# Kernel tuning notes

Measured on AMD Instinct MI355X. Metric: run time of the kernel, lower is better.

## Reference

```python
import jax, jax.numpy as jnp
import numpy as np

N_NODES = 100000
N_EDGES = 3200000
D = 64
NEG_SLOPE = 0.01  # torch F.leaky_relu default


def setup_inputs() -> dict:
    key = jax.random.key(0)
    ks = jax.random.split(key, 7)
    s = 1.0 / np.sqrt(D)
    x = jax.random.normal(ks[0], (N_NODES, D), jnp.float32)
    src = jax.random.randint(ks[1], (N_EDGES,), 0, N_NODES)
    dst = jax.random.randint(ks[2], (N_EDGES,), 0, N_NODES)
    W1a = jax.random.normal(ks[3], (D, D), jnp.float32) * s
    W2a = jax.random.normal(ks[4], (D, D), jnp.float32) * s
    W1b = jax.random.normal(ks[5], (D, D), jnp.float32) * s
    W2b = jax.random.normal(ks[6], (D, D), jnp.float32) * s
    return {"x": x, "W1a": W1a, "W2a": W2a, "W1b": W1b, "W2b": W2b,
            "src": src, "dst": dst}


def _ngcf_conv(x, src, dst, norm, W1, W2):
    # message: norm_ij * (W1 x_j + W2 (x_j (*) x_i)), aggregated at dst i,
    # plus self-transform W1 x_i  (NGCF propagation rule, pre-activation)
    xs = x[src]            # [E, D] gather of neighbor feats
    xd = x[dst]            # [E, D] gather of center feats
    msg = norm[:, None] * (xs @ W1 + (xs * xd) @ W2)   # [E, D]
    agg = jax.ops.segment_sum(msg, dst, num_segments=x.shape[0])
    return x @ W1 + agg


def reference(x, W1a, W2a, W1b, W2b, src, dst):
    n = x.shape[0]
    ones = jnp.ones(src.shape[0], x.dtype)
    deg = jnp.maximum(jax.ops.segment_sum(ones, dst, num_segments=n), 1.0)
    norm = jax.lax.rsqrt(deg[src] * deg[dst])          # 1/sqrt(d_j d_i)
    h1 = jax.nn.leaky_relu(_ngcf_conv(x, src, dst, norm, W1a, W2a), NEG_SLOPE)
    h2 = jax.nn.leaky_relu(_ngcf_conv(h1, src, dst, norm, W1b, W2b), NEG_SLOPE)
    h3 = _ngcf_conv(h2, src, dst, norm, W1b, W2b)      # no activation (matches source)
    return jnp.concatenate([h1, h2, h3], axis=-1)      # [N, 3*D]
```

## Files before the change

kernel.cpp:

```cpp
#include <hip/hip_runtime.h>
#include <hip/hip_bf16.h>

#define N_NODES 100000
#define N_EDGES 3200000
#define D 64
#define NEG_SLOPE 0.01f

#define B_SHIFT 9
#define NB ((N_NODES + 511) >> B_SHIFT)
#define T_EDGES 4096
#define NBIN ((N_EDGES + T_EDGES - 1) / T_EDGES)

using bf16x8 = __attribute__((ext_vector_type(8))) short;
using f32x4  = __attribute__((ext_vector_type(4))) float;

__device__ __forceinline__ unsigned short f2bf(float f) {
    __hip_bfloat16 h = __float2bfloat16(f);
    return *reinterpret_cast<unsigned short*>(&h);
}
__device__ __forceinline__ float bflo(unsigned int u) { return __uint_as_float(u << 16); }
__device__ __forceinline__ float bfhi(unsigned int u) { return __uint_as_float(u & 0xffff0000u); }
__device__ __forceinline__ float bf2f(unsigned short h) { return __uint_as_float(((unsigned int)h) << 16); }

__global__ __launch_bounds__(256) void bhist_k(const int* __restrict__ dst, int* __restrict__ btot) {
    __shared__ int hist[NB];
    int tid = threadIdx.x;
    for (int b = tid; b < NB; b += 256) hist[b] = 0;
    __syncthreads();
    int e0 = blockIdx.x * T_EDGES;
    int e1 = min(e0 + T_EDGES, N_EDGES);
    for (int e = e0 + tid; e < e1; e += 256) atomicAdd(&hist[dst[e] >> B_SHIFT], 1);
    __syncthreads();
    for (int b = tid; b < NB; b += 256) {
        int h = hist[b];
        if (h) atomicAdd(&btot[b], h);
    }
}

__global__ __launch_bounds__(256) void bscan_k(const int* __restrict__ btot, int* __restrict__ bbase) {
    __shared__ int wsum[4];
    int t = threadIdx.x;
    int lane = t & 63, w = t >> 6;
    int v = (t < NB) ? btot[t] : 0;
    int incl = v;
    #pragma unroll
    for (int o = 1; o < 64; o <<= 1) {
        int u = __shfl_up(incl, o, 64);
        if (lane >= o) incl += u;
    }
    if (lane == 63) wsum[w] = incl;
    __syncthreads();
    int woff = 0;
    for (int k = 0; k < w; ++k) woff += wsum[k];
    if (t < NB) bbase[t] = woff + incl - v;
    if (t == NB) bbase[NB] = N_EDGES;
}

__global__ __launch_bounds__(256) void bucket_k(const int* __restrict__ src, const int* __restrict__ dst,
                                                const int* __restrict__ bbase, int* __restrict__ bcnt2,
                                                unsigned* __restrict__ pairs) {
    __shared__ int hist[NB];
    __shared__ int lbase[NB];
    __shared__ int lcnt[NB];
    __shared__ int gbase[NB];
    __shared__ int wsum[4];
    __shared__ unsigned buf[T_EDGES];
    int tid = threadIdx.x;
    for (int b = tid; b < NB; b += 256) { hist[b] = 0; lcnt[b] = 0; }
    __syncthreads();
    int e0 = blockIdx.x * T_EDGES;
    int e1 = min(e0 + T_EDGES, N_EDGES);
    for (int e = e0 + tid; e < e1; e += 256) atomicAdd(&hist[dst[e] >> B_SHIFT], 1);
    __syncthreads();
    {
        int v = (tid < NB) ? hist[tid] : 0;
        int lane = tid & 63, w = tid >> 6;
        int incl = v;
        #pragma unroll
        for (int o = 1; o < 64; o <<= 1) {
            int u = __shfl_up(incl, o, 64);
            if (lane >= o) incl += u;
        }
        if (lane == 63) wsum[w] = incl;
        __syncthreads();
        int woff = 0;
        for (int k = 0; k < w; ++k) woff += wsum[k];
        if (tid < NB) {
            int excl = woff + incl - v;
            lbase[tid] = excl;
            int p = v ? atomicAdd(&bcnt2[tid], v) : 0;
            gbase[tid] = bbase[tid] + p - excl;
        }
    }
    __syncthreads();
    for (int e = e0 + tid; e < e1; e += 256) {
        int sv = src[e], dv = dst[e];
        int b = dv >> B_SHIFT;
        int loc = lbase[b] + atomicAdd(&lcnt[b], 1);
        buf[loc] = ((unsigned)sv << 9) | (unsigned)(dv & 511);
    }
    __syncthreads();
    int n = e1 - e0;
    for (int i = tid; i < n; i += 256) {
        unsigned pr = buf[i];
        int lo = 0, hi = NB - 1;
        while (lo < hi) { int mid = (lo + hi + 1) >> 1; if (lbase[mid] <= i) lo = mid; else hi = mid - 1; }
        pairs[gbase[lo] + i] = pr;
    }
}

__global__ __launch_bounds__(512) void fine_k(const unsigned* __restrict__ pairs, const int* __restrict__ bbase,
                                              int* __restrict__ degi, int* __restrict__ offs,
                                              float* __restrict__ rsd, int* __restrict__ csr_src,
                                              const float* __restrict__ x, unsigned short* __restrict__ xb) {
    __shared__ int cnt[512];
    __shared__ int offl[512];
    __shared__ int wsum[8];
    __shared__ float rsdl[256];
    int b = blockIdx.x >> 1, half = blockIdx.x & 1, t = threadIdx.x;
    int start = bbase[b];
    int end = bbase[b + 1];
    cnt[t] = 0;
    __syncthreads();
    for (int e = start + t; e < end; e += 512) atomicAdd(&cnt[pairs[e] & 511], 1);
    __syncthreads();
    int d = cnt[t];
    int lane = t & 63, w = t >> 6;
    int incl = d;
    #pragma unroll
    for (int o = 1; o < 64; o <<= 1) {
        int u = __shfl_up(incl, o, 64);
        if (lane >= o) incl += u;
    }
    if (lane == 63) wsum[w] = incl;
    __syncthreads();
    int woff = 0;
    for (int k = 0; k < w; ++k) woff += wsum[k];
    int myoff = start + woff + incl - d;
    offl[t] = myoff;
    int n = (b << B_SHIFT) + t;
    float rn = rsqrtf((float)(d > 0 ? d : 1));
    if ((t >> 8) == half) {
        if (n < N_NODES) {
            degi[n] = d;
            offs[n] = myoff;
            rsd[n] = rn;
        }
        rsdl[t & 255] = rn;
    }
    cnt[t] = 0;
    __syncthreads();
    for (int e = start + t; e < end; e += 512) {
        unsigned pr = pairs[e];
        int li = pr & 511;
        if ((li >> 8) == half) {
            int p = atomicAdd(&cnt[li], 1);
            csr_src[offl[li] + p] = (int)(pr >> 9);
        }
    }
    __syncthreads();
    int nbase = (b << B_SHIFT) + (half << 8);
    for (int i = t; i < 256 * 16; i += 512) {
        int nl = i >> 4;
        int node = nbase + nl;
        if (node < N_NODES) {
            float r = rsdl[nl];
            float4 v = ((const float4*)x)[(size_t)node * 16 + (i & 15)];
            unsigned int lo = ((unsigned int)f2bf(r * v.y) << 16) | f2bf(r * v.x);
            unsigned int hi = ((unsigned int)f2bf(r * v.w) << 16) | f2bf(r * v.z);
            ((uint2*)xb)[(size_t)node * 16 + (i & 15)] = make_uint2(lo, hi);
        }
    }
}

__global__ __launch_bounds__(256) void agg_k(const unsigned short* __restrict__ xb,
                                             const float* __restrict__ rsd,
                                             const int* __restrict__ offs, const int* __restrict__ degi,
                                             const int* __restrict__ csr_src, float* __restrict__ s) {
    int node = blockIdx.x * 4 + (threadIdx.x >> 6);
    if (node >= N_NODES) return;
    int lane = threadIdx.x & 63;
    int g = lane >> 3;
    int q = lane & 7;
    int start = offs[node];
    int deg = degi[node];
    const uint4* in4 = (const uint4*)xb;
    float acc0 = 0.f, acc1 = 0.f, acc2 = 0.f, acc3 = 0.f;
    float acc4 = 0.f, acc5 = 0.f, acc6 = 0.f, acc7 = 0.f;
    for (int base = 0; base < deg; base += 64) {
        int m = min(deg - base, 64);
        int idxv = csr_src[start + base + min(lane, m - 1)];
        for (int j = 0; j < m; j += 32) {
            int e0 = j + g, e1 = j + 8 + g, e2 = j + 16 + g, e3 = j + 24 + g;
            bool v0 = e0 < m, v1 = e1 < m, v2 = e2 < m, v3 = e3 < m;
            int s0 = __shfl(idxv, e0, 64);
            int s1 = __shfl(idxv, v1 ? e1 : 0, 64);
            int s2 = __shfl(idxv, v2 ? e2 : 0, 64);
            int s3 = __shfl(idxv, v3 ? e3 : 0, 64);
            uint4 p0 = in4[(size_t)s0 * 8 + q];
            uint4 p1 = in4[(size_t)s1 * 8 + q];
            uint4 p2 = in4[(size_t)s2 * 8 + q];
            uint4 p3 = in4[(size_t)s3 * 8 + q];
            float w0 = v0 ? 1.f : 0.f, w1 = v1 ? 1.f : 0.f;
            float w2 = v2 ? 1.f : 0.f, w3 = v3 ? 1.f : 0.f;
            acc0 += w0 * bflo(p0.x); acc1 += w0 * bfhi(p0.x);
            acc2 += w0 * bflo(p0.y); acc3 += w0 * bfhi(p0.y);
            acc4 += w0 * bflo(p0.z); acc5 += w0 * bfhi(p0.z);
            acc6 += w0 * bflo(p0.w); acc7 += w0 * bfhi(p0.w);
            acc0 += w1 * bflo(p1.x); acc1 += w1 * bfhi(p1.x);
            acc2 += w1 * bflo(p1.y); acc3 += w1 * bfhi(p1.y);
            acc4 += w1 * bflo(p1.z); acc5 += w1 * bfhi(p1.z);
            acc6 += w1 * bflo(p1.w); acc7 += w1 * bfhi(p1.w);
            acc0 += w2 * bflo(p2.x); acc1 += w2 * bfhi(p2.x);
            acc2 += w2 * bflo(p2.y); acc3 += w2 * bfhi(p2.y);
            acc4 += w2 * bflo(p2.z); acc5 += w2 * bfhi(p2.z);
            acc6 += w2 * bflo(p2.w); acc7 += w2 * bfhi(p2.w);
            acc0 += w3 * bflo(p3.x); acc1 += w3 * bfhi(p3.x);
            acc2 += w3 * bflo(p3.y); acc3 += w3 * bfhi(p3.y);
            acc4 += w3 * bflo(p3.z); acc5 += w3 * bfhi(p3.z);
            acc6 += w3 * bflo(p3.w); acc7 += w3 * bfhi(p3.w);
        }
    }
    #pragma unroll
    for (int off = 8; off < 64; off <<= 1) {
        acc0 += __shfl_xor(acc0, off, 64); acc1 += __shfl_xor(acc1, off, 64);
        acc2 += __shfl_xor(acc2, off, 64); acc3 += __shfl_xor(acc3, off, 64);
        acc4 += __shfl_xor(acc4, off, 64); acc5 += __shfl_xor(acc5, off, 64);
        acc6 += __shfl_xor(acc6, off, 64); acc7 += __shfl_xor(acc7, off, 64);
    }
    if (g == 0) {
        float rn = rsd[node];
        float4 r0, r1;
        r0.x = rn * acc0; r0.y = rn * acc1; r0.z = rn * acc2; r0.w = rn * acc3;
        r1.x = rn * acc4; r1.y = rn * acc5; r1.z = rn * acc6; r1.w = rn * acc7;
        ((float4*)s)[node * 16 + q * 2]     = r0;
        ((float4*)s)[node * 16 + q * 2 + 1] = r1;
    }
}

__global__ __launch_bounds__(256) void comb_k(const float* __restrict__ in, int stride,
                                              const float* __restrict__ s,
                                              const float* __restrict__ W1, const float* __restrict__ W2,
                                              float* __restrict__ out, int act,
                                              unsigned short* __restrict__ hb, const float* __restrict__ rsd,
                                              int bfout) {
    int tid = threadIdx.x;
    int w = tid >> 6;
    int l = tid & 63;
    int lr = l & 15;
    int lk = l >> 4;

    bf16x8 w1h[2], w1l[2], w2h[2], w2l[2];
    #pragma unroll
    for (int s2 = 0; s2 < 2; ++s2) {
        #pragma unroll
        for (int i = 0; i < 8; ++i) {
            int k = s2 * 32 + lk * 8 + i;
            float v1 = W1[k * D + w * 16 + lr];
            float v2 = W2[k * D + w * 16 + lr];
            unsigned short h1 = f2bf(v1);
            unsigned short h2 = f2bf(v2);
            w1h[s2][i] = (short)h1; w1l[s2][i] = (short)f2bf(v1 - bf2f(h1));
            w2h[s2][i] = (short)h2; w2l[s2][i] = (short)f2bf(v2 - bf2f(h2));
        }
    }

    int n0 = blockIdx.x * 32;
    bf16x8 ah[2][2], al[2][2], bh[2][2], bl[2][2];
    #pragma unroll
    for (int rt = 0; rt < 2; ++rt) {
        int n = n0 + rt * 16 + lr;
        const float* ip = in + (size_t)n * stride + lk * 8;
        const float* sp = s + (size_t)n * D + lk * 8;
        #pragma unroll
        for (int s2 = 0; s2 < 2; ++s2) {
            float ia[8], sa[8];
            *(float4*)&ia[0] = *(const float4*)(ip + s2 * 32);
            *(float4*)&ia[4] = *(const float4*)(ip + s2 * 32 + 4);
            *(float4*)&sa[0] = *(const float4*)(sp + s2 * 32);
            *(float4*)&sa[4] = *(const float4*)(sp + s2 * 32 + 4);
            #pragma unroll
            for (int i = 0; i < 8; ++i) {
                float a = ia[i] + sa[i];
                float b = sa[i] * ia[i];
                unsigned short hA = f2bf(a);
                unsigned short hB = f2bf(b);
                ah[rt][s2][i] = (short)hA; al[rt][s2][i] = (short)f2bf(a - bf2f(hA));
                bh[rt][s2][i] = (short)hB; bl[rt][s2][i] = (short)f2bf(b - bf2f(hB));
            }
        }
    }

    f32x4 acc[2] = {{0.f, 0.f, 0.f, 0.f}, {0.f, 0.f, 0.f, 0.f}};
    #pragma unroll
    for (int rt = 0; rt < 2; ++rt) {
        #pragma unroll
        for (int s2 = 0; s2 < 2; ++s2) {
            acc[rt] = __builtin_amdgcn_mfma_f32_16x16x32_bf16(ah[rt][s2], w1h[s2], acc[rt], 0, 0, 0);
            acc[rt] = __builtin_amdgcn_mfma_f32_16x16x32_bf16(al[rt][s2], w1h[s2], acc[rt], 0, 0, 0);
            acc[rt] = __builtin_amdgcn_mfma_f32_16x16x32_bf16(ah[rt][s2], w1l[s2], acc[rt], 0, 0, 0);
            acc[rt] = __builtin_amdgcn_mfma_f32_16x16x32_bf16(bh[rt][s2], w2h[s2], acc[rt], 0, 0, 0);
            acc[rt] = __builtin_amdgcn_mfma_f32_16x16x32_bf16(bl[rt][s2], w2h[s2], acc[rt], 0, 0, 0);
            acc[rt] = __builtin_amdgcn_mfma_f32_16x16x32_bf16(bh[rt][s2], w2l[s2], acc[rt], 0, 0, 0);
        }
    }

    #pragma unroll
    for (int rt = 0; rt < 2; ++rt) {
        #pragma unroll
        for (int r = 0; r < 4; ++r) {
            int n = n0 + rt * 16 + lk * 4 + r;
            float v = acc[rt][r];
            if (act) v = v >= 0.f ? v : NEG_SLOPE * v;
            out[(size_t)n * 192 + w * 16 + lr] = v;
            if (bfout) hb[(size_t)n * D + w * 16 + lr] = f2bf(rsd[n] * v);
        }
    }
}

extern "C" void kernel_launch(void* const* d_in, const int* in_sizes, int n_in,
                              void* d_out, int out_size, void* d_ws, size_t ws_size,
                              hipStream_t stream) {
    const float* x   = (const float*)d_in[0];
    const float* W1a = (const float*)d_in[1];
    const float* W2a = (const float*)d_in[2];
    const float* W1b = (const float*)d_in[3];
    const float* W2b = (const float*)d_in[4];
    const int*   src = (const int*)d_in[5];
    const int*   dst = (const int*)d_in[6];
    float* out = (float*)d_out;

    int*   btot    = (int*)d_ws;
    int*   bcnt2   = btot + 256;
    int*   bbase   = bcnt2 + 256;
    int*   degi    = bbase + 256;
    int*   offs    = degi + N_NODES;
    float* rsd     = (float*)(offs + N_NODES);
    int*   csr_src = (int*)(rsd + N_NODES);
    unsigned* pairs = (unsigned*)(csr_src + N_EDGES);
    unsigned short* xb = (unsigned short*)(pairs + N_EDGES);
    unsigned short* hb = (unsigned short*)pairs;
    float* s       = (float*)(xb + (size_t)N_NODES * D);

    hipMemsetAsync(btot, 0, 512 * sizeof(int), stream);

    bhist_k<<<NBIN, 256, 0, stream>>>(dst, btot);
    bscan_k<<<1, 256, 0, stream>>>(btot, bbase);
    bucket_k<<<NBIN, 256, 0, stream>>>(src, dst, bbase, bcnt2, pairs);
    fine_k<<<NB * 2, 512, 0, stream>>>(pairs, bbase, degi, offs, rsd, csr_src, x, xb);

    int ab = (N_NODES + 3) / 4;
    int cbg = N_NODES / 32;

    agg_k<<<ab, 256, 0, stream>>>(xb, rsd, offs, degi, csr_src, s);
    comb_k<<<cbg, 256, 0, stream>>>(x, D, s, W1a, W2a, out + 0, 1, hb, rsd, 1);
    agg_k<<<ab, 256, 0, stream>>>(hb, rsd, offs, degi, csr_src, s);
    comb_k<<<cbg, 256, 0, stream>>>(out + 0, 192, s, W1b, W2b, out + 64, 1, hb, rsd, 1);
    agg_k<<<ab, 256, 0, stream>>>(hb, rsd, offs, degi, csr_src, s);
    comb_k<<<cbg, 256, 0, stream>>>(out + 64, 192, s, W1b, W2b, out + 128, 0, hb, rsd, 0);
}
```

Before: 458.3 us.

## Drop global histogram pass using fixed-capacity buckets; unroll aggregation gather

Removes the separate bucket histogram kernel by scattering edge pairs into fixed-capacity per-bucket regions (BCAP slots each) and scanning the per-bucket counts afterwards. This saves one full read of dst. Fine binning now reads pairs from those capacity-strided regions. Bucket_k stores each pair's bucket id in shared memory instead of binary-searching it at write-out, and agg_k issues eight gathers per 64-edge chunk instead of looping in groups of four. The risks are overflow if a bucket exceeds BCAP edges, and that pairs now shares memory with the s buffer.

```diff
diff --git a/kernel.cpp b/kernel.cpp
--- a/kernel.cpp
+++ b/kernel.cpp
@@ -8,6 +8,7 @@
 
 #define B_SHIFT 9
 #define NB ((N_NODES + 511) >> B_SHIFT)
+#define BCAP 18432
 #define T_EDGES 4096
 #define NBIN ((N_EDGES + T_EDGES - 1) / T_EDGES)
 
@@ -22,42 +23,8 @@
 __device__ __forceinline__ float bfhi(unsigned int u) { return __uint_as_float(u & 0xffff0000u); }
 __device__ __forceinline__ float bf2f(unsigned short h) { return __uint_as_float(((unsigned int)h) << 16); }
 
-__global__ __launch_bounds__(256) void bhist_k(const int* __restrict__ dst, int* __restrict__ btot) {
-    __shared__ int hist[NB];
-    int tid = threadIdx.x;
-    for (int b = tid; b < NB; b += 256) hist[b] = 0;
-    __syncthreads();
-    int e0 = blockIdx.x * T_EDGES;
-    int e1 = min(e0 + T_EDGES, N_EDGES);
-    for (int e = e0 + tid; e < e1; e += 256) atomicAdd(&hist[dst[e] >> B_SHIFT], 1);
-    __syncthreads();
-    for (int b = tid; b < NB; b += 256) {
-        int h = hist[b];
-        if (h) atomicAdd(&btot[b], h);
-    }
-}
-
-__global__ __launch_bounds__(256) void bscan_k(const int* __restrict__ btot, int* __restrict__ bbase) {
-    __shared__ int wsum[4];
-    int t = threadIdx.x;
-    int lane = t & 63, w = t >> 6;
-    int v = (t < NB) ? btot[t] : 0;
-    int incl = v;
-    #pragma unroll
-    for (int o = 1; o < 64; o <<= 1) {
-        int u = __shfl_up(incl, o, 64);
-        if (lane >= o) incl += u;
-    }
-    if (lane == 63) wsum[w] = incl;
-    __syncthreads();
-    int woff = 0;
-    for (int k = 0; k < w; ++k) woff += wsum[k];
-    if (t < NB) bbase[t] = woff + incl - v;
-    if (t == NB) bbase[NB] = N_EDGES;
-}
-
 __global__ __launch_bounds__(256) void bucket_k(const int* __restrict__ src, const int* __restrict__ dst,
-                                                const int* __restrict__ bbase, int* __restrict__ bcnt2,
+                                                int* __restrict__ bcnt2,
                                                 unsigned* __restrict__ pairs) {
     __shared__ int hist[NB];
     __shared__ int lbase[NB];
@@ -65,6 +32,7 @@
     __shared__ int gbase[NB];
     __shared__ int wsum[4];
     __shared__ unsigned buf[T_EDGES];
+    __shared__ unsigned char bid[T_EDGES];
     int tid = threadIdx.x;
     for (int b = tid; b < NB; b += 256) { hist[b] = 0; lcnt[b] = 0; }
     __syncthreads();
@@ -89,7 +57,7 @@
             int excl = woff + incl - v;
             lbase[tid] = excl;
             int p = v ? atomicAdd(&bcnt2[tid], v) : 0;
-            gbase[tid] = bbase[tid] + p - excl;
+            gbase[tid] = tid * BCAP + p - excl;
         }
     }
     __syncthreads();
@@ -98,18 +66,37 @@
         int b = dv >> B_SHIFT;
         int loc = lbase[b] + atomicAdd(&lcnt[b], 1);
         buf[loc] = ((unsigned)sv << 9) | (unsigned)(dv & 511);
+        bid[loc] = (unsigned char)b;
     }
     __syncthreads();
     int n = e1 - e0;
     for (int i = tid; i < n; i += 256) {
-        unsigned pr = buf[i];
-        int lo = 0, hi = NB - 1;
-        while (lo < hi) { int mid = (lo + hi + 1) >> 1; if (lbase[mid] <= i) lo = mid; else hi = mid - 1; }
-        pairs[gbase[lo] + i] = pr;
-    }
-}
-
-__global__ __launch_bounds__(512) void fine_k(const unsigned* __restrict__ pairs, const int* __restrict__ bbase,
+        int b = bid[i];
+        pairs[gbase[b] + i] = buf[i];
+    }
+}
+
+__global__ __launch_bounds__(256) void bscan_k(const int* __restrict__ bcnt2, int* __restrict__ bbase) {
+    __shared__ int wsum[4];
+    int t = threadIdx.x;
+    int lane = t & 63, w = t >> 6;
+    int v = (t < NB) ? bcnt2[t] : 0;
+    int incl = v;
+    #pragma unroll
+    for (int o = 1; o < 64; o <<= 1) {
+        int u = __shfl_up(incl, o, 64);
+        if (lane >= o) incl += u;
+    }
+    if (lane == 63) wsum[w] = incl;
+    __syncthreads();
+    int woff = 0;
+    for (int k = 0; k < w; ++k) woff += wsum[k];
+    if (t < NB) bbase[t] = woff + incl - v;
+    if (t == NB) bbase[NB] = N_EDGES;
+}
+
+__global__ __launch_bounds__(512) void fine_k(const unsigned* __restrict__ pairs,
+                                              const int* __restrict__ bcnt2, const int* __restrict__ bbase,
                                               int* __restrict__ degi, int* __restrict__ offs,
                                               float* __restrict__ rsd, int* __restrict__ csr_src,
                                               const float* __restrict__ x, unsigned short* __restrict__ xb) {
@@ -118,11 +105,12 @@
     __shared__ int wsum[8];
     __shared__ float rsdl[256];
     int b = blockIdx.x >> 1, half = blockIdx.x & 1, t = threadIdx.x;
-    int start = bbase[b];
-    int end = bbase[b + 1];
+    int pstart = b * BCAP;
+    int pend = pstart + bcnt2[b];
+    int cbase = bbase[b];
     cnt[t] = 0;
     __syncthreads();
-    for (int e = start + t; e < end; e += 512) atomicAdd(&cnt[pairs[e] & 511], 1);
+    for (int e = pstart + t; e < pend; e += 512) atomicAdd(&cnt[pairs[e] & 511], 1);
     __syncthreads();
     int d = cnt[t];
     int lane = t & 63, w = t >> 6;
@@ -136,7 +124,7 @@
     __syncthreads();
     int woff = 0;
     for (int k = 0; k < w; ++k) woff += wsum[k];
-    int myoff = start + woff + incl - d;
+    int myoff = cbase + woff + incl - d;
     offl[t] = myoff;
     int n = (b << B_SHIFT) + t;
     float rn = rsqrtf((float)(d > 0 ? d : 1));
@@ -150,7 +138,7 @@
     }
     cnt[t] = 0;
     __syncthreads();
-    for (int e = start + t; e < end; e += 512) {
+    for (int e = pstart + t; e < pend; e += 512) {
         unsigned pr = pairs[e];
         int li = pr & 511;
         if ((li >> 8) == half) {
@@ -172,6 +160,12 @@
         }
     }
 }
+
+#define ACC8(P, W) \
+    acc0 += W * bflo(P.x); acc1 += W * bfhi(P.x); \
+    acc2 += W * bflo(P.y); acc3 += W * bfhi(P.y); \
+    acc4 += W * bflo(P.z); acc5 += W * bfhi(P.z); \
+    acc6 += W * bflo(P.w); acc7 += W * bfhi(P.w);
 
 __global__ __launch_bounds__(256) void agg_k(const unsigned short* __restrict__ xb,
                                              const float* __restrict__ rsd,
@@ -190,35 +184,33 @@
     for (int base = 0; base < deg; base += 64) {
         int m = min(deg - base, 64);
         int idxv = csr_src[start + base + min(lane, m - 1)];
-        for (int j = 0; j < m; j += 32) {
-            int e0 = j + g, e1 = j + 8 + g, e2 = j + 16 + g, e3 = j + 24 + g;
-            bool v0 = e0 < m, v1 = e1 < m, v2 = e2 < m, v3 = e3 < m;
-            int s0 = __shfl(idxv, e0, 64);
-            int s1 = __shfl(idxv, v1 ? e1 : 0, 64);
-            int s2 = __shfl(idxv, v2 ? e2 : 0, 64);
-            int s3 = __shfl(idxv, v3 ? e3 : 0, 64);
-            uint4 p0 = in4[(size_t)s0 * 8 + q];
-            uint4 p1 = in4[(size_t)s1 * 8 + q];
-            uint4 p2 = in4[(size_t)s2 * 8 + q];
-            uint4 p3 = in4[(size_t)s3 * 8 + q];
-            float w0 = v0 ? 1.f : 0.f, w1 = v1 ? 1.f : 0.f;
-            float w2 = v2 ? 1.f : 0.f, w3 = v3 ? 1.f : 0.f;
-            acc0 += w0 * bflo(p0.x); acc1 += w0 * bfhi(p0.x);
-            acc2 += w0 * bflo(p0.y); acc3 += w0 * bfhi(p0.y);
-            acc4 += w0 * bflo(p0.z); acc5 += w0 * bfhi(p0.z);
-            acc6 += w0 * bflo(p0.w); acc7 += w0 * bfhi(p0.w);
-            acc0 += w1 * bflo(p1.x); acc1 += w1 * bfhi(p1.x);
-            acc2 += w1 * bflo(p1.y); acc3 += w1 * bfhi(p1.y);
-            acc4 += w1 * bflo(p1.z); acc5 += w1 * bfhi(p1.z);
-            acc6 += w1 * bflo(p1.w); acc7 += w1 * bfhi(p1.w);
-            acc0 += w2 * bflo(p2.x); acc1 += w2 * bfhi(p2.x);
-            acc2 += w2 * bflo(p2.y); acc3 += w2 * bfhi(p2.y);
-            acc4 += w2 * bflo(p2.z); acc5 += w2 * bfhi(p2.z);
-            acc6 += w2 * bflo(p2.w); acc7 += w2 * bfhi(p2.w);
-            acc0 += w3 * bflo(p3.x); acc1 += w3 * bfhi(p3.x);
-            acc2 += w3 * bflo(p3.y); acc3 += w3 * bfhi(p3.y);
-            acc4 += w3 * bflo(p3.z); acc5 += w3 * bfhi(p3.z);
-            acc6 += w3 * bflo(p3.w); acc7 += w3 * bfhi(p3.w);
+        int e0 = g, e1 = 8 + g, e2 = 16 + g, e3 = 24 + g;
+        int s0 = __shfl(idxv, e0, 64);
+        int s1 = __shfl(idxv, e1, 64);
+        int s2 = __shfl(idxv, e2, 64);
+        int s3 = __shfl(idxv, e3, 64);
+        uint4 p0 = in4[(size_t)s0 * 8 + q];
+        uint4 p1 = in4[(size_t)s1 * 8 + q];
+        uint4 p2 = in4[(size_t)s2 * 8 + q];
+        uint4 p3 = in4[(size_t)s3 * 8 + q];
+        float w0 = (e0 < m) ? 1.f : 0.f, w1 = (e1 < m) ? 1.f : 0.f;
+        float w2 = (e2 < m) ? 1.f : 0.f, w3 = (e3 < m) ? 1.f : 0.f;
+        if (m > 32) {
+            int e4 = 32 + g, e5 = 40 + g, e6 = 48 + g, e7 = 56 + g;
+            int s4 = __shfl(idxv, e4, 64);
+            int s5 = __shfl(idxv, e5, 64);
+            int s6 = __shfl(idxv, e6, 64);
+            int s7 = __shfl(idxv, e7, 64);
+            uint4 p4 = in4[(size_t)s4 * 8 + q];
+            uint4 p5 = in4[(size_t)s5 * 8 + q];
+            uint4 p6 = in4[(size_t)s6 * 8 + q];
+            uint4 p7 = in4[(size_t)s7 * 8 + q];
+            float w4 = (e4 < m) ? 1.f : 0.f, w5 = (e5 < m) ? 1.f : 0.f;
+            float w6 = (e6 < m) ? 1.f : 0.f, w7 = (e7 < m) ? 1.f : 0.f;
+            ACC8(p0, w0) ACC8(p1, w1) ACC8(p2, w2) ACC8(p3, w3)
+            ACC8(p4, w4) ACC8(p5, w5) ACC8(p6, w6) ACC8(p7, w7)
+        } else {
+            ACC8(p0, w0) ACC8(p1, w1) ACC8(p2, w2) ACC8(p3, w3)
         }
     }
     #pragma unroll
@@ -330,24 +322,22 @@
     const int*   dst = (const int*)d_in[6];
     float* out = (float*)d_out;
 
-    int*   btot    = (int*)d_ws;
-    int*   bcnt2   = btot + 256;
+    int*   bcnt2   = (int*)d_ws;
     int*   bbase   = bcnt2 + 256;
     int*   degi    = bbase + 256;
     int*   offs    = degi + N_NODES;
     float* rsd     = (float*)(offs + N_NODES);
     int*   csr_src = (int*)(rsd + N_NODES);
-    unsigned* pairs = (unsigned*)(csr_src + N_EDGES);
-    unsigned short* xb = (unsigned short*)(pairs + N_EDGES);
-    unsigned short* hb = (unsigned short*)pairs;
-    float* s       = (float*)(xb + (size_t)N_NODES * D);
-
-    hipMemsetAsync(btot, 0, 512 * sizeof(int), stream);
-
-    bhist_k<<<NBIN, 256, 0, stream>>>(dst, btot);
-    bscan_k<<<1, 256, 0, stream>>>(btot, bbase);
-    bucket_k<<<NBIN, 256, 0, stream>>>(src, dst, bbase, bcnt2, pairs);
-    fine_k<<<NB * 2, 512, 0, stream>>>(pairs, bbase, degi, offs, rsd, csr_src, x, xb);
+    unsigned short* xb = (unsigned short*)(csr_src + N_EDGES);
+    unsigned short* hb = xb + (size_t)N_NODES * D;
+    float* s       = (float*)(hb + (size_t)N_NODES * D);
+    unsigned* pairs = (unsigned*)s;
+
+    hipMemsetAsync(bcnt2, 0, 256 * sizeof(int), stream);
+
+    bucket_k<<<NBIN, 256, 0, stream>>>(src, dst, bcnt2, pairs);
+    bscan_k<<<1, 256, 0, stream>>>(bcnt2, bbase);
+    fine_k<<<NB * 2, 512, 0, stream>>>(pairs, bcnt2, bbase, degi, offs, rsd, csr_src, x, xb);
 
     int ab = (N_NODES + 3) / 4;
     int cbg = N_NODES / 32;
```

Result: no change. 459.4 us (+0.2%).
